# Kernel tuning notes

Hardware: AMD Instinct MI355X
Metric: run time of the kernel (lower is better)

## Reference

```python
import jax, jax.numpy as jnp
import numpy as np

HIDDEN = 2048
NUM_HEADS = 32
NUM_KV_HEADS = 8
HEAD_DIM = 128
EPS = 1e-6
ROPE_BASE = 10000.0
T = 2048


def setup_inputs() -> dict:
    key = jax.random.key(0)
    k1, k2, k3, k4, k5 = jax.random.split(key, 5)
    q_size = NUM_HEADS * HEAD_DIM
    kv_size = NUM_KV_HEADS * HEAD_DIM
    s = 0.02
    return {
        "positions": jnp.arange(T, dtype=jnp.int32),
        "hidden_states": jax.random.normal(k1, (T, HIDDEN), dtype=jnp.float32),
        "wqkv": jax.random.normal(k2, (q_size + 2 * kv_size, HIDDEN), dtype=jnp.float32) * s,
        "wo": jax.random.normal(k3, (HIDDEN, q_size), dtype=jnp.float32) * s,
        "q_norm_w": jnp.ones((HEAD_DIM,), dtype=jnp.float32),
        "k_norm_w": jnp.ones((HEAD_DIM,), dtype=jnp.float32),
    }


def _rms_norm(x, w, eps=EPS):
    # x: [T, H, D]; normalize over last dim
    var = jnp.mean(jnp.square(x), axis=-1, keepdims=True)
    return x * jax.lax.rsqrt(var + eps) * w


def _rope(positions, x):
    # neox-style rotate-half RoPE. x: [T, H, D]
    half = HEAD_DIM // 2
    inv_freq = 1.0 / (ROPE_BASE ** (jnp.arange(0, half, dtype=jnp.float32) / half))
    ang = positions.astype(jnp.float32)[:, None] * inv_freq  # [T, half]
    cos = jnp.cos(ang)[:, None, :]  # [T, 1, half]
    sin = jnp.sin(ang)[:, None, :]
    x1, x2 = x[..., :half], x[..., half:]
    return jnp.concatenate([x1 * cos - x2 * sin, x2 * cos + x1 * sin], axis=-1)


def reference(positions, hidden_states, wqkv, wo, q_norm_w, k_norm_w):
    q_size = NUM_HEADS * HEAD_DIM
    kv_size = NUM_KV_HEADS * HEAD_DIM
    scaling = HEAD_DIM ** -0.5

    qkv = hidden_states @ wqkv.T  # [T, q_size + 2*kv_size]
    q = qkv[:, :q_size].reshape(-1, NUM_HEADS, HEAD_DIM)
    k = qkv[:, q_size:q_size + kv_size].reshape(-1, NUM_KV_HEADS, HEAD_DIM)
    v = qkv[:, q_size + kv_size:].reshape(-1, NUM_KV_HEADS, HEAD_DIM)

    q = _rms_norm(q, q_norm_w)
    k = _rms_norm(k, k_norm_w)
    q = _rope(positions, q)
    k = _rope(positions, k)

    # GQA: repeat kv heads to match query heads
    group = NUM_HEADS // NUM_KV_HEADS
    k = jnp.repeat(k, group, axis=1)  # [T, H, D]
    v = jnp.repeat(v, group, axis=1)

    scores = jnp.einsum("thd,shd->hts", q, k) * scaling  # [H, T, T]
    causal = positions[:, None] >= positions[None, :]  # [T, T]
    scores = jnp.where(causal[None], scores, jnp.finfo(scores.dtype).min)
    probs = jax.nn.softmax(scores, axis=-1)
    o = jnp.einsum("hts,shd->thd", probs, v)  # [T, H, D]
    return o.reshape(-1, q_size) @ wo.T  # [T, HIDDEN]
```

## Files before the change

kernel.cpp:

```cpp
#include <hip/hip_runtime.h>
#include <hip/hip_bf16.h>

#define T_SEQ   2048
#define HIDDEN  2048
#define NUM_H   32
#define NUM_KV  8
#define HD      128
#define Q_SIZE  4096
#define QKV_N   6144

typedef __bf16 bf16;
typedef __bf16 bf16x8 __attribute__((ext_vector_type(8)));
typedef __bf16 bf16x4 __attribute__((ext_vector_type(4)));
typedef float  floatx4 __attribute__((ext_vector_type(4)));

#define GLOBAL_AS(p) ((const __attribute__((address_space(1))) void*)(p))
#define LDS_AS(p)    ((__attribute__((address_space(3))) void*)(p))

#define BARRIER() do { asm volatile("" ::: "memory"); \
                       __builtin_amdgcn_s_barrier();  \
                       asm volatile("" ::: "memory"); } while (0)

__global__ void detect_dtype(const unsigned short* __restrict__ wq, int* flagp)
{
    const int lane = threadIdx.x;
    int cnt = 0;
    for (int i = lane; i < 512; i += 64) {
        int ef = (wq[i] >> 7) & 0xFF;
        if (ef >= 90 && ef <= 130) cnt++;
    }
    #pragma unroll
    for (int m = 32; m; m >>= 1) cnt += __shfl_xor(cnt, m);
    if (lane == 0) *flagp = (cnt >= 430) ? 1 : 0;
}

__global__ __launch_bounds__(256) void convert_all(
    const void* __restrict__ h, const void* __restrict__ wq,
    const void* __restrict__ wo_, const void* __restrict__ qn,
    const void* __restrict__ kn,
    bf16* __restrict__ hb, bf16* __restrict__ wqb, bf16* __restrict__ wob,
    bf16* __restrict__ qnb, bf16* __restrict__ knb, const int* flagp)
{
    long e = ((long)blockIdx.x * 256 + threadIdx.x) * 8;
    const void* src; bf16* dst; long off;
    if      (e < 4194304)  { src = h;   dst = hb;  off = e; }
    else if (e < 16777216) { src = wq;  dst = wqb; off = e - 4194304; }
    else if (e < 25165824) { src = wo_; dst = wob; off = e - 16777216; }
    else if (e < 25165952) { src = qn;  dst = qnb; off = e - 25165824; }
    else if (e < 25166080) { src = kn;  dst = knb; off = e - 25165952; }
    else return;

    if (*flagp) {
        *(bf16x8*)(dst + off) = *(const bf16x8*)((const bf16*)src + off);
    } else {
        const float* f = (const float*)src + off;
        bf16x8 v;
        #pragma unroll
        for (int i = 0; i < 8; ++i) v[i] = (bf16)f[i];
        *(bf16x8*)(dst + off) = v;
    }
}

__global__ __launch_bounds__(512, 2) void gemm8p(
    const bf16* __restrict__ A, const bf16* __restrict__ B,
    bf16* __restrict__ C, int N, int K, int lda, int ldb)
{
    __shared__ bf16 As[2][2][128 * 64];
    __shared__ bf16 Bs[2][2][128 * 64];

    const int tid  = threadIdx.x;
    const int wave = tid >> 6, lane = tid & 63;
    const int quad = lane >> 4, l16 = lane & 15;
    const int wm = wave >> 2;
    const int wn = wave & 3;
    const int wh = wn >> 1;
    const int bro = (wn & 1) * 64;
    const long baseM = (long)blockIdx.x * 256;
    const long baseN = (long)blockIdx.y * 256;

    auto stage = [&](int p, int t) {
        const long kc = (long)t * 64;
        #pragma unroll
        for (int l = 0; l < 8; ++l) {
            const int h   = (l >> 1) & 1;
            const int n0  = (l & 1) * 512 + wave * 64;
            const int n   = n0 + lane;
            const int row = n >> 3, slot = n & 7;
            const int gc  = (slot ^ (row & 7)) * 8;
            if (l < 4)
                __builtin_amdgcn_global_load_lds(
                    GLOBAL_AS(A + (baseM + h * 128 + row) * (long)lda + kc + gc),
                    LDS_AS(&As[p][h][n0 * 8]), 16, 0, 0);
            else
                __builtin_amdgcn_global_load_lds(
                    GLOBAL_AS(B + (baseN + h * 128 + row) * (long)ldb + kc + gc),
                    LDS_AS(&Bs[p][h][n0 * 8]), 16, 0, 0);
        }
    };

    floatx4 acc[8][4] = {};

    stage(0, 0);

    const int NT = K / 64;
    for (int t = 0; t < NT; ++t) {
        const int p = t & 1;
        if (t + 1 < NT) {
            stage(p ^ 1, t + 1);
            asm volatile("s_waitcnt vmcnt(8)" ::: "memory");
        } else {
            asm volatile("s_waitcnt vmcnt(0)" ::: "memory");
        }
        __builtin_amdgcn_sched_barrier(0);
        BARRIER();

        const bf16* Aw = &As[p][wm][0];
        const bf16* Bw = &Bs[p][wh][0];

        bf16x8 af[4][2], bf0[2][2], bf1[2][2];

        #pragma unroll
        for (int mf = 0; mf < 4; ++mf)
            #pragma unroll
            for (int ks = 0; ks < 2; ++ks) {
                const int r = mf * 16 + l16;
                af[mf][ks] = *(const bf16x8*)(Aw + r * 64 + (((ks * 4 + quad) ^ (r & 7)) * 8));
            }
        #pragma unroll
        for (int nf = 0; nf < 2; ++nf)
            #pragma unroll
            for (int ks = 0; ks < 2; ++ks) {
                const int r = bro + nf * 16 + l16;
                bf0[nf][ks] = *(const bf16x8*)(Bw + r * 64 + (((ks * 4 + quad) ^ (r & 7)) * 8));
            }
        __builtin_amdgcn_s_setprio(1);
        #pragma unroll
        for (int mf = 0; mf < 4; ++mf)
            #pragma unroll
            for (int nf = 0; nf < 2; ++nf)
                #pragma unroll
                for (int ks = 0; ks < 2; ++ks)
                    acc[mf][nf] = __builtin_amdgcn_mfma_f32_16x16x32_bf16(af[mf][ks], bf0[nf][ks], acc[mf][nf], 0, 0, 0);
        __builtin_amdgcn_s_setprio(0);

        #pragma unroll
        for (int nf = 0; nf < 2; ++nf)
            #pragma unroll
            for (int ks = 0; ks < 2; ++ks) {
                const int r = bro + (nf + 2) * 16 + l16;
                bf1[nf][ks] = *(const bf16x8*)(Bw + r * 64 + (((ks * 4 + quad) ^ (r & 7)) * 8));
            }
        __builtin_amdgcn_s_setprio(1);
        #pragma unroll
        for (int mf = 0; mf < 4; ++mf)
            #pragma unroll
            for (int nf = 0; nf < 2; ++nf)
                #pragma unroll
                for (int ks = 0; ks < 2; ++ks)
                    acc[mf][nf + 2] = __builtin_amdgcn_mfma_f32_16x16x32_bf16(af[mf][ks], bf1[nf][ks], acc[mf][nf + 2], 0, 0, 0);
        __builtin_amdgcn_s_setprio(0);

        #pragma unroll
        for (int mf = 0; mf < 4; ++mf)
            #pragma unroll
            for (int ks = 0; ks < 2; ++ks) {
                const int r = (mf + 4) * 16 + l16;
                af[mf][ks] = *(const bf16x8*)(Aw + r * 64 + (((ks * 4 + quad) ^ (r & 7)) * 8));
            }
        __builtin_amdgcn_s_setprio(1);
        #pragma unroll
        for (int mf = 0; mf < 4; ++mf)
            #pragma unroll
            for (int nf = 0; nf < 2; ++nf)
                #pragma unroll
                for (int ks = 0; ks < 2; ++ks)
                    acc[mf + 4][nf] = __builtin_amdgcn_mfma_f32_16x16x32_bf16(af[mf][ks], bf0[nf][ks], acc[mf + 4][nf], 0, 0, 0);
        __builtin_amdgcn_s_setprio(0);

        __builtin_amdgcn_s_setprio(1);
        #pragma unroll
        for (int mf = 0; mf < 4; ++mf)
            #pragma unroll
            for (int nf = 0; nf < 2; ++nf)
                #pragma unroll
                for (int ks = 0; ks < 2; ++ks)
                    acc[mf + 4][nf + 2] = __builtin_amdgcn_mfma_f32_16x16x32_bf16(af[mf][ks], bf1[nf][ks], acc[mf + 4][nf + 2], 0, 0, 0);
        __builtin_amdgcn_s_setprio(0);

        BARRIER();
    }

    #pragma unroll
    for (int i = 0; i < 8; ++i)
        #pragma unroll
        for (int j = 0; j < 4; ++j)
            #pragma unroll
            for (int r = 0; r < 4; ++r) {
                long row = baseM + wm * 128 + i * 16 + quad * 4 + r;
                long col = baseN + wn * 64 + j * 16 + l16;
                C[row * (long)N + col] = (bf16)acc[i][j][r];
            }
}

__global__ __launch_bounds__(256) void gemm_db(
    const bf16* __restrict__ A, const bf16* __restrict__ B,
    float* __restrict__ Cp, int N, int Kd, int lda, int ldb)
{
    __shared__ bf16 As[2][128 * 32];
    __shared__ bf16 Bs[2][128 * 32];

    const int tid  = threadIdx.x;
    const int wave = tid >> 6, lane = tid & 63;
    const int quad = lane >> 4, l16 = lane & 15;
    const int wm = (wave & 1) * 64, wn = (wave >> 1) * 64;
    const long baseM = (long)blockIdx.x * 128;
    const long baseN = (long)blockIdx.y * 128;
    const long koff  = (long)blockIdx.z * Kd;

    const int  srow = wave * 16 + (lane >> 2);
    const int  scol = (lane & 3) * 8;
    const long aoff0 = (baseM + srow) * (long)lda + koff + scol;
    const long aoff1 = (baseM + 64 + srow) * (long)lda + koff + scol;
    const long boff0 = (baseN + srow) * (long)ldb + koff + scol;
    const long boff1 = (baseN + 64 + srow) * (long)ldb + koff + scol;
    const int  lds0 = wave * 512;
    const int  lds1 = 2048 + wave * 512;

    auto stage = [&](int p, int k0) {
        __builtin_amdgcn_global_load_lds(GLOBAL_AS(A + aoff0 + k0), LDS_AS(As[p] + lds0), 16, 0, 0);
        __builtin_amdgcn_global_load_lds(GLOBAL_AS(A + aoff1 + k0), LDS_AS(As[p] + lds1), 16, 0, 0);
        __builtin_amdgcn_global_load_lds(GLOBAL_AS(B + boff0 + k0), LDS_AS(Bs[p] + lds0), 16, 0, 0);
        __builtin_amdgcn_global_load_lds(GLOBAL_AS(B + boff1 + k0), LDS_AS(Bs[p] + lds1), 16, 0, 0);
    };

    floatx4 acc[4][4] = {};

    stage(0, 0);
    asm volatile("s_waitcnt vmcnt(0)" ::: "memory");
    __builtin_amdgcn_s_barrier();

    int cur = 0;
    for (int k0 = 0; k0 < Kd; k0 += 32) {
        if (k0 + 32 < Kd) stage(cur ^ 1, k0 + 32);
        __builtin_amdgcn_sched_barrier(0);

        bf16x8 af[4], bfr[4];
        #pragma unroll
        for (int i = 0; i < 4; ++i)
            af[i] = *(const bf16x8*)(As[cur] + (wm + i * 16 + l16) * 32 + quad * 8);
        #pragma unroll
        for (int j = 0; j < 4; ++j)
            bfr[j] = *(const bf16x8*)(Bs[cur] + (wn + j * 16 + l16) * 32 + quad * 8);

        #pragma unroll
        for (int i = 0; i < 4; ++i)
            #pragma unroll
            for (int j = 0; j < 4; ++j)
                acc[i][j] = __builtin_amdgcn_mfma_f32_16x16x32_bf16(af[i], bfr[j], acc[i][j], 0, 0, 0);

        asm volatile("s_waitcnt vmcnt(0)" ::: "memory");
        __builtin_amdgcn_s_barrier();
        cur ^= 1;
    }

    const long Mrows = (long)gridDim.x * 128;
    float* C = Cp + (long)blockIdx.z * Mrows * N;
    #pragma unroll
    for (int i = 0; i < 4; ++i)
        #pragma unroll
        for (int j = 0; j < 4; ++j)
            #pragma unroll
            for (int r = 0; r < 4; ++r) {
                long row = baseM + wm + i * 16 + quad * 4 + r;
                long col = baseN + wn + j * 16 + l16;
                C[row * (long)N + col] = acc[i][j][r];
            }
}

__global__ __launch_bounds__(256) void reduce2(
    const float* __restrict__ P0, const float* __restrict__ P1,
    void* __restrict__ out, const int* flagp)
{
    long i = ((long)blockIdx.x * 256 + threadIdx.x) * 4;
    floatx4 a = *(const floatx4*)(P0 + i);
    floatx4 b = *(const floatx4*)(P1 + i);
    floatx4 s = a + b;
    if (*flagp) {
        bf16x4 o;
        #pragma unroll
        for (int r = 0; r < 4; ++r) o[r] = (bf16)s[r];
        *(bf16x4*)((bf16*)out + i) = o;
    } else {
        *(floatx4*)((float*)out + i) = s;
    }
}

__global__ __launch_bounds__(256) void qkv_post(
    bf16* __restrict__ qkv, const int* __restrict__ positions,
    const bf16* __restrict__ qnw, const bf16* __restrict__ knw)
{
    const int t = blockIdx.x;
    const int tid = threadIdx.x, wave = tid >> 6, lane = tid & 63;
    const float pos = (float)positions[t];

    const float inv = expf(-(float)lane * (float)(9.210340371976184 / 64.0));
    float sn, cs;
    sincosf(pos * inv, &sn, &cs);

    bf16* row = qkv + (long)t * QKV_N;

    for (int u = wave; u < 40; u += 4) {
        bf16* p       = (u < 32) ? row + u * HD : row + Q_SIZE + (u - 32) * HD;
        const bf16* w = (u < 32) ? qnw : knw;
        float x1 = (float)p[lane], x2 = (float)p[lane + 64];
        float ss = x1 * x1 + x2 * x2;
        #pragma unroll
        for (int m = 32; m; m >>= 1) ss += __shfl_xor(ss, m);
        float rr = rsqrtf(ss * (1.f / 128.f) + 1e-6f);
        float y1 = x1 * rr * (float)w[lane];
        float y2 = x2 * rr * (float)w[lane + 64];
        p[lane]      = (bf16)(y1 * cs - y2 * sn);
        p[lane + 64] = (bf16)(y2 * cs + y1 * sn);
    }
}

__global__ __launch_bounds__(256) void vtrans(const bf16* __restrict__ qkv,
                                              bf16* __restrict__ vt)
{
    __shared__ bf16 tile[64][136];
    const int t0 = blockIdx.x * 64, kvh = blockIdx.y, tid = threadIdx.x;

    const int rl = tid >> 4, c8 = (tid & 15) * 8;
    const bf16* src = qkv + (long)t0 * QKV_N + 5120 + kvh * HD;
    #pragma unroll
    for (int it = 0; it < 4; ++it) {
        int r = it * 16 + rl;
        *(bf16x8*)(&tile[r][c8]) = *(const bf16x8*)(src + (long)r * QKV_N + c8);
    }
    __syncthreads();

    const int d = tid >> 1, tb = (tid & 1) * 32;
    bf16* dst = vt + ((long)kvh * HD + d) * T_SEQ + t0 + tb;
    #pragma unroll
    for (int it = 0; it < 4; ++it) {
        bf16x8 v;
        #pragma unroll
        for (int j = 0; j < 8; ++j) v[j] = tile[tb + it * 8 + j][d];
        *(bf16x8*)(dst + it * 8) = v;
    }
}

__global__ __launch_bounds__(256, 3) void attn5(bf16* qkv, const bf16* __restrict__ vt)
{
    __shared__ bf16 Ks[2][64 * 128];
    __shared__ bf16 Vs[128 * 64];

    const int tid  = threadIdx.x, wave = tid >> 6, lane = tid & 63;
    const int quad = lane >> 4, l16 = lane & 15;
    const int h = blockIdx.x, kvh = h >> 2;
    const int iq = 31 - blockIdx.y;
    const int q0 = iq * 64;

    const float C1 = 0.12753236f;
    const float C2 = 17.312340f;

    bf16x8 qf[4];
    {
        const bf16* qa = qkv + (long)(q0 + wave * 16 + l16) * QKV_N + h * HD + quad * 8;
        #pragma unroll
        for (int ks = 0; ks < 4; ++ks) qf[ks] = *(const bf16x8*)(qa + ks * 32);
    }

    floatx4 oacc[8] = {};
    float ls = 0.f;

    const int krl = lane >> 4, kc = lane & 15;
    const int vrl = lane >> 3, vc = lane & 7;
    const int kswz = (kc ^ (wave * 4 + krl)) * 8;
    const int vswz = (vc ^ (vrl & 7)) * 8;
    const int wsig = ((wave & 1) << 1) | (wave >> 1);
    const int sq4  = (((quad & 1) << 1) | (quad >> 1)) << 2;

    const bf16* kg0 = qkv + Q_SIZE + kvh * HD;
    const bf16* vg0 = vt + (long)kvh * HD * T_SEQ;

    auto stageK = [&](int p, int kt) {
        const bf16* kg = kg0 + (long)(kt * 64) * QKV_N;
        #pragma unroll
        for (int it = 0; it < 4; ++it) {
            const int rK = it * 16 + wsig * 4 + krl;
            __builtin_amdgcn_global_load_lds(GLOBAL_AS(kg + (long)rK * QKV_N + kswz),
                                             LDS_AS(&Ks[p][it * 2048 + wave * 512]), 16, 0, 0);
        }
    };
    auto stageV = [&](int kt) {
        const bf16* vg = vg0 + kt * 64;
        #pragma unroll
        for (int it = 0; it < 4; ++it) {
            const int dV = it * 32 + wave * 8 + vrl;
            __builtin_amdgcn_global_load_lds(GLOBAL_AS(vg + (long)dV * T_SEQ + vswz),
                                             LDS_AS(&Vs[it * 2048 + wave * 512]), 16, 0, 0);
        }
    };

    stageK(0, 0);

    const int qg = q0 + wave * 16 + l16;

    for (int kt = 0; kt <= iq; ++kt) {
        const int p = kt & 1;
        __syncthreads();
        stageV(kt);
        if (kt < iq) stageK(p ^ 1, kt + 1);

        const int k0 = kt * 64;

        floatx4 sT[4] = {};
        #pragma unroll
        for (int j2 = 0; j2 < 4; ++j2)
            #pragma unroll
            for (int ks = 0; ks < 4; ++ks) {
                bf16x8 kf = *(const bf16x8*)(&Ks[p][(j2 * 16 + l16) * 128 + (((ks * 4 + quad) ^ l16) * 8)]);
                sT[j2] = __builtin_amdgcn_mfma_f32_16x16x32_bf16(kf, qf[ks], sT[j2], 0, 0, 0);
            }

        const bool diag = (kt == iq);
        unsigned lov[4], hiv[4];
        #pragma unroll
        for (int j2 = 0; j2 < 4; ++j2) {
            float ev[4];
            #pragma unroll
            for (int r = 0; r < 4; ++r) {
                float x = __builtin_amdgcn_exp2f(sT[j2][r] * C1 - C2);
                if (diag && (k0 + j2 * 16 + sq4 + r > qg)) x = 0.f;
                ls += x;
                ev[r] = x;
            }
            asm("v_cvt_pk_bf16_f32 %0, %1, %2" : "=v"(lov[j2]) : "v"(ev[0]), "v"(ev[1]));
            asm("v_cvt_pk_bf16_f32 %0, %1, %2" : "=v"(hiv[j2]) : "v"(ev[2]), "v"(ev[3]));
        }

        bf16x8 pa[2];
        #pragma unroll
        for (int ks2 = 0; ks2 < 2; ++ks2) {
            auto wl = __builtin_amdgcn_permlane32_swap(lov[2 * ks2], lov[2 * ks2 + 1], false, false);
            auto wh = __builtin_amdgcn_permlane32_swap(hiv[2 * ks2], hiv[2 * ks2 + 1], false, false);
            union { unsigned w[4]; bf16x8 v; } u;
            u.w[0] = wl[0]; u.w[1] = wh[0]; u.w[2] = wl[1]; u.w[3] = wh[1];
            pa[ks2] = u.v;
        }

        if (kt < iq) asm volatile("s_waitcnt vmcnt(4)" ::: "memory");
        else         asm volatile("s_waitcnt vmcnt(0)" ::: "memory");
        __builtin_amdgcn_s_barrier();
        __builtin_amdgcn_sched_barrier(0);

        #pragma unroll
        for (int ks2 = 0; ks2 < 2; ++ks2)
            #pragma unroll
            for (int vj = 0; vj < 8; ++vj) {
                const int d = vj * 16 + l16;
                bf16x8 vb = *(const bf16x8*)(&Vs[d * 64 + (((ks2 * 4 + quad) ^ (d & 7)) * 8)]);
                oacc[vj] = __builtin_amdgcn_mfma_f32_16x16x32_bf16(pa[ks2], vb, oacc[vj], 0, 0, 0);
            }
    }

    ls += __shfl_xor(ls, 16); ls += __shfl_xor(ls, 32);
    float rinv[4];
    #pragma unroll
    for (int r = 0; r < 4; ++r) rinv[r] = 1.f / __shfl(ls, quad * 4 + r);

    #pragma unroll
    for (int vj = 0; vj < 8; ++vj)
        #pragma unroll
        for (int r = 0; r < 4; ++r) {
            const long row = q0 + wave * 16 + quad * 4 + r;
            qkv[row * (long)QKV_N + h * HD + vj * 16 + l16] = (bf16)(oacc[vj][r] * rinv[r]);
        }
}

extern "C" void kernel_launch(void* const* d_in, const int* in_sizes, int n_in,
                              void* d_out, int out_size, void* d_ws, size_t ws_size,
                              hipStream_t stream)
{
    const int* positions = (const int*)d_in[0];

    char* ws = (char*)d_ws;
    bf16* qkv  = (bf16*)(ws);
    bf16* hb   = (bf16*)(ws + 25165824);
    bf16* vt   = hb;
    float* P0  = (float*)(ws + 25165824);
    float* P1  = (float*)(ws + 41943040);
    bf16* wqb  = (bf16*)(ws + 33554432);
    bf16* wob  = (bf16*)(ws + 58720256);
    bf16* qnb  = (bf16*)(ws + 75497472);
    bf16* knb  = (bf16*)(ws + 75497728);
    int*  flag = (int*) (ws + 75497984);

    detect_dtype<<<dim3(1), dim3(64), 0, stream>>>((const unsigned short*)d_in[2], flag);
    convert_all<<<dim3(12289), dim3(256), 0, stream>>>(
        d_in[1], d_in[2], d_in[3], d_in[4], d_in[5],
        hb, wqb, wob, qnb, knb, flag);

    gemm8p<<<dim3(T_SEQ / 256, QKV_N / 256), dim3(512), 0, stream>>>(
        hb, wqb, qkv, QKV_N, HIDDEN, HIDDEN, HIDDEN);
    vtrans<<<dim3(T_SEQ / 64, NUM_KV), dim3(256), 0, stream>>>(qkv, vt);
    qkv_post<<<dim3(T_SEQ), dim3(256), 0, stream>>>(qkv, positions, qnb, knb);
    attn5<<<dim3(NUM_H, 32), dim3(256), 0, stream>>>(qkv, vt);
    gemm_db<<<dim3(T_SEQ / 128, HIDDEN / 128, 2), dim3(256), 0, stream>>>(
        qkv, wob, P0, HIDDEN, Q_SIZE / 2, QKV_N, Q_SIZE);
    reduce2<<<dim3(4096), dim3(256), 0, stream>>>(P0, P1, d_out, flag);
}
```

Before: 329.6 us.

## Interleave fine-grained global-to-LDS staging with MFMA phases in QKV GEMM

Restructures the QKV projection GEMM's main loop into an 8-phase, 2-tile-unrolled schedule. Each phase issues a small slice of the next tile's global-to-LDS loads between LDS fragment reads and MFMA groups, with precise vmcnt waits and barriers, so memory traffic is spread across compute instead of issued in one burst per tile. The grid is also swapped so blockIdx.x walks the N (weight) dimension, which changes which tiles run together and how they share cache. The cost is many more barriers per tile and a fragile hand-tuned waitcnt schedule.

```diff
diff --git a/kernel.cpp b/kernel.cpp
--- a/kernel.cpp
+++ b/kernel.cpp
@@ -20,6 +20,10 @@
 #define BARRIER() do { asm volatile("" ::: "memory"); \
                        __builtin_amdgcn_s_barrier();  \
                        asm volatile("" ::: "memory"); } while (0)
+#define VMCNT0() asm volatile("s_waitcnt vmcnt(0)" ::: "memory")
+#define VMCNT2() asm volatile("s_waitcnt vmcnt(2)" ::: "memory")
+#define VMCNT4() asm volatile("s_waitcnt vmcnt(4)" ::: "memory")
+#define VMCNT6() asm volatile("s_waitcnt vmcnt(6)" ::: "memory")
 
 __global__ void detect_dtype(const unsigned short* __restrict__ wq, int* flagp)
 {
@@ -75,64 +79,60 @@
     const int wn = wave & 3;
     const int wh = wn >> 1;
     const int bro = (wn & 1) * 64;
-    const long baseM = (long)blockIdx.x * 256;
-    const long baseN = (long)blockIdx.y * 256;
-
-    auto stage = [&](int p, int t) {
+    const long baseN = (long)blockIdx.x * 256;
+    const long baseM = (long)blockIdx.y * 256;
+
+    const int sr  = tid >> 3;
+    const int sgc = ((tid & 7) ^ (sr & 7)) * 8;
+
+    auto stagePB = [&](int p, int h, int t) {
         const long kc = (long)t * 64;
-        #pragma unroll
-        for (int l = 0; l < 8; ++l) {
-            const int h   = (l >> 1) & 1;
-            const int n0  = (l & 1) * 512 + wave * 64;
-            const int n   = n0 + lane;
-            const int row = n >> 3, slot = n & 7;
-            const int gc  = (slot ^ (row & 7)) * 8;
-            if (l < 4)
-                __builtin_amdgcn_global_load_lds(
-                    GLOBAL_AS(A + (baseM + h * 128 + row) * (long)lda + kc + gc),
-                    LDS_AS(&As[p][h][n0 * 8]), 16, 0, 0);
-            else
-                __builtin_amdgcn_global_load_lds(
-                    GLOBAL_AS(B + (baseN + h * 128 + row) * (long)ldb + kc + gc),
-                    LDS_AS(&Bs[p][h][n0 * 8]), 16, 0, 0);
-        }
+        const bf16* src = B + (baseN + h * 128 + sr) * (long)ldb + kc + sgc;
+        __builtin_amdgcn_global_load_lds(GLOBAL_AS(src),
+            LDS_AS(&Bs[p][h][wave * 512]), 16, 0, 0);
+        __builtin_amdgcn_global_load_lds(GLOBAL_AS(src + 64 * (long)ldb),
+            LDS_AS(&Bs[p][h][4096 + wave * 512]), 16, 0, 0);
+    };
+    auto stagePA = [&](int p, int g, int t) {
+        const long kc = (long)t * 64;
+        const bf16* src = A + (baseM + g * 64 + sr) * (long)lda + kc + sgc;
+        __builtin_amdgcn_global_load_lds(GLOBAL_AS(src),
+            LDS_AS(&As[p][0][g * 4096 + wave * 512]), 16, 0, 0);
+        __builtin_amdgcn_global_load_lds(GLOBAL_AS(src + 128 * (long)lda),
+            LDS_AS(&As[p][1][g * 4096 + wave * 512]), 16, 0, 0);
     };
 
     floatx4 acc[8][4] = {};
-
-    stage(0, 0);
-
-    const int NT = K / 64;
-    for (int t = 0; t < NT; ++t) {
-        const int p = t & 1;
-        if (t + 1 < NT) {
-            stage(p ^ 1, t + 1);
-            asm volatile("s_waitcnt vmcnt(8)" ::: "memory");
-        } else {
-            asm volatile("s_waitcnt vmcnt(0)" ::: "memory");
-        }
-        __builtin_amdgcn_sched_barrier(0);
-        BARRIER();
-
-        const bf16* Aw = &As[p][wm][0];
-        const bf16* Bw = &Bs[p][wh][0];
-
-        bf16x8 af[4][2], bf0[2][2], bf1[2][2];
-
+    bf16x8 af[4][2], bf0[2][2], bf1[2][2];
+
+    auto rdAf = [&](int p, int g) {
         #pragma unroll
         for (int mf = 0; mf < 4; ++mf)
             #pragma unroll
             for (int ks = 0; ks < 2; ++ks) {
-                const int r = mf * 16 + l16;
-                af[mf][ks] = *(const bf16x8*)(Aw + r * 64 + (((ks * 4 + quad) ^ (r & 7)) * 8));
-            }
+                const int r = g * 64 + mf * 16 + l16;
+                af[mf][ks] = *(const bf16x8*)(&As[p][wm][r * 64 + (((ks * 4 + quad) ^ (r & 7)) * 8)]);
+            }
+    };
+    auto rdB0 = [&](int p) {
         #pragma unroll
         for (int nf = 0; nf < 2; ++nf)
             #pragma unroll
             for (int ks = 0; ks < 2; ++ks) {
                 const int r = bro + nf * 16 + l16;
-                bf0[nf][ks] = *(const bf16x8*)(Bw + r * 64 + (((ks * 4 + quad) ^ (r & 7)) * 8));
-            }
+                bf0[nf][ks] = *(const bf16x8*)(&Bs[p][wh][r * 64 + (((ks * 4 + quad) ^ (r & 7)) * 8)]);
+            }
+    };
+    auto rdB1 = [&](int p) {
+        #pragma unroll
+        for (int nf = 0; nf < 2; ++nf)
+            #pragma unroll
+            for (int ks = 0; ks < 2; ++ks) {
+                const int r = bro + (nf + 2) * 16 + l16;
+                bf1[nf][ks] = *(const bf16x8*)(&Bs[p][wh][r * 64 + (((ks * 4 + quad) ^ (r & 7)) * 8)]);
+            }
+    };
+    auto mmQ = [&](int mo, int no, bf16x8 (&bfr)[2][2]) {
         __builtin_amdgcn_s_setprio(1);
         #pragma unroll
         for (int mf = 0; mf < 4; ++mf)
@@ -140,53 +140,59 @@
             for (int nf = 0; nf < 2; ++nf)
                 #pragma unroll
                 for (int ks = 0; ks < 2; ++ks)
-                    acc[mf][nf] = __builtin_amdgcn_mfma_f32_16x16x32_bf16(af[mf][ks], bf0[nf][ks], acc[mf][nf], 0, 0, 0);
+                    acc[mo + mf][no + nf] = __builtin_amdgcn_mfma_f32_16x16x32_bf16(
+                        af[mf][ks], bfr[nf][ks], acc[mo + mf][no + nf], 0, 0, 0);
         __builtin_amdgcn_s_setprio(0);
-
-        #pragma unroll
-        for (int nf = 0; nf < 2; ++nf)
-            #pragma unroll
-            for (int ks = 0; ks < 2; ++ks) {
-                const int r = bro + (nf + 2) * 16 + l16;
-                bf1[nf][ks] = *(const bf16x8*)(Bw + r * 64 + (((ks * 4 + quad) ^ (r & 7)) * 8));
-            }
-        __builtin_amdgcn_s_setprio(1);
-        #pragma unroll
-        for (int mf = 0; mf < 4; ++mf)
-            #pragma unroll
-            for (int nf = 0; nf < 2; ++nf)
-                #pragma unroll
-                for (int ks = 0; ks < 2; ++ks)
-                    acc[mf][nf + 2] = __builtin_amdgcn_mfma_f32_16x16x32_bf16(af[mf][ks], bf1[nf][ks], acc[mf][nf + 2], 0, 0, 0);
-        __builtin_amdgcn_s_setprio(0);
-
-        #pragma unroll
-        for (int mf = 0; mf < 4; ++mf)
-            #pragma unroll
-            for (int ks = 0; ks < 2; ++ks) {
-                const int r = (mf + 4) * 16 + l16;
-                af[mf][ks] = *(const bf16x8*)(Aw + r * 64 + (((ks * 4 + quad) ^ (r & 7)) * 8));
-            }
-        __builtin_amdgcn_s_setprio(1);
-        #pragma unroll
-        for (int mf = 0; mf < 4; ++mf)
-            #pragma unroll
-            for (int nf = 0; nf < 2; ++nf)
-                #pragma unroll
-                for (int ks = 0; ks < 2; ++ks)
-                    acc[mf + 4][nf] = __builtin_amdgcn_mfma_f32_16x16x32_bf16(af[mf][ks], bf0[nf][ks], acc[mf + 4][nf], 0, 0, 0);
-        __builtin_amdgcn_s_setprio(0);
-
-        __builtin_amdgcn_s_setprio(1);
-        #pragma unroll
-        for (int mf = 0; mf < 4; ++mf)
-            #pragma unroll
-            for (int nf = 0; nf < 2; ++nf)
-                #pragma unroll
-                for (int ks = 0; ks < 2; ++ks)
-                    acc[mf + 4][nf + 2] = __builtin_amdgcn_mfma_f32_16x16x32_bf16(af[mf][ks], bf1[nf][ks], acc[mf + 4][nf + 2], 0, 0, 0);
-        __builtin_amdgcn_s_setprio(0);
-
+    };
+
+    stagePB(0, 0, 0); stagePB(0, 1, 0); stagePA(0, 0, 0); stagePA(0, 1, 0);
+    stagePB(1, 0, 1);
+    VMCNT2();
+    BARRIER();
+
+    const int NT2 = K / 128;
+    for (int j = 0; j < NT2; ++j) {
+        const int t1 = 2 * j + 1;
+        const bool more = (j + 1 < NT2);
+
+        rdAf(0, 0); rdB0(0);
+        stagePB(1, 1, t1);
+        BARRIER(); __builtin_amdgcn_sched_barrier(0);
+        mmQ(0, 0, bf0);
+        BARRIER();
+        rdB1(0);
+        stagePA(1, 0, t1);
+        VMCNT6();
+        BARRIER(); __builtin_amdgcn_sched_barrier(0);
+        mmQ(0, 2, bf1);
+        BARRIER();
+        rdAf(0, 1);
+        stagePA(1, 1, t1);
+        BARRIER(); __builtin_amdgcn_sched_barrier(0);
+        mmQ(4, 0, bf0);
+        BARRIER();
+        if (more) { stagePB(0, 0, t1 + 1); VMCNT4(); } else { VMCNT2(); }
+        BARRIER(); __builtin_amdgcn_sched_barrier(0);
+        mmQ(4, 2, bf1);
+        BARRIER();
+        rdAf(1, 0); rdB0(1);
+        if (more) stagePB(0, 1, t1 + 1);
+        BARRIER(); __builtin_amdgcn_sched_barrier(0);
+        mmQ(0, 0, bf0);
+        BARRIER();
+        rdB1(1);
+        if (more) { stagePA(0, 0, t1 + 1); VMCNT6(); } else { VMCNT0(); }
+        BARRIER(); __builtin_amdgcn_sched_barrier(0);
+        mmQ(0, 2, bf1);
+        BARRIER();
+        rdAf(1, 1);
+        if (more) stagePA(0, 1, t1 + 1);
+        BARRIER(); __builtin_amdgcn_sched_barrier(0);
+        mmQ(4, 0, bf0);
+        BARRIER();
+        if (more) { stagePB(1, 0, t1 + 2); VMCNT4(); }
+        BARRIER(); __builtin_amdgcn_sched_barrier(0);
+        mmQ(4, 2, bf1);
         BARRIER();
     }
 
@@ -502,7 +508,7 @@
         d_in[1], d_in[2], d_in[3], d_in[4], d_in[5],
         hb, wqb, wob, qnb, knb, flag);
 
-    gemm8p<<<dim3(T_SEQ / 256, QKV_N / 256), dim3(512), 0, stream>>>(
+    gemm8p<<<dim3(QKV_N / 256, T_SEQ / 256), dim3(512), 0, stream>>>(
         hb, wqb, qkv, QKV_N, HIDDEN, HIDDEN, HIDDEN);
     vtrans<<<dim3(T_SEQ / 64, NUM_KV), dim3(256), 0, stream>>>(qkv, vt);
     qkv_post<<<dim3(T_SEQ), dim3(256), 0, stream>>>(qkv, positions, qnb, knb);
```

After: 324.4 us. No clear change (-1.6%).
